# Kernel optimization log

Hardware: AMD Instinct MI355X
Metric: run time of the kernel (lower is better)

## Reference

```python
import jax, jax.numpy as jnp
import numpy as np

D_K = 64

def setup_inputs() -> dict:
    key = jax.random.key(0)
    kq, kk, kv, kw = jax.random.split(key, 4)
    B, H, L, Dk, Dv = 16, 8, 1024, 64, 64
    Q = jax.random.normal(kq, (B, H, L, Dk), dtype=jnp.float32)
    K = jax.random.normal(kk, (B, H, L, Dk), dtype=jnp.float32)
    V = jax.random.normal(kv, (B, H, L, Dv), dtype=jnp.float32)
    W = jax.random.normal(kw, (H, L, 2 * Dk), dtype=jnp.float32)
    return {"Q": Q, "K": K, "V": V, "W": W}

def reference(Q, K, V, W):
    scale = 1.0 / jnp.sqrt(jnp.float32(D_K))
    # branch 1: standard scaled dot-product attention scores [B,H,Lq,Lk]
    scores = jnp.einsum('bhqd,bhkd->bhqk', Q, K) * scale
    attn = jax.nn.softmax(scores, axis=-1)
    # branch 2: learned-weight concat(Q,K) projection
    # W [H, Lq, 2Dk] @ cat(Q,K)^T [B,H,2Dk,Lk] -> [B,H,Lq,Lk]
    qk = jnp.concatenate([Q, K], axis=-1)  # [B,H,L,2Dk]
    scores_cat = jnp.einsum('hqc,bhkc->bhqk', W, qk) * scale
    attn_cat = jax.nn.softmax(scores_cat, axis=-1)
    attention = attn + attn_cat
    context = jnp.einsum('bhqk,bhkd->bhqd', attention, V)
    return context, attention
```

## Files before the change

### kernel.cpp

```cpp
#include <hip/hip_runtime.h>

#define L_SEQ 1024
#define DKV 64
#define NT 16

typedef float f32x4 __attribute__((ext_vector_type(4)));
typedef _Float16 f16x8 __attribute__((ext_vector_type(8)));
typedef _Float16 f16x4 __attribute__((ext_vector_type(4)));

#define QK_STRIDE 136
#define VT_STRIDE 72
#define ATT_STRIDE 72

__device__ __forceinline__ f32x4 mfma16(f16x8 a, f16x8 b, f32x4 c) {
    return __builtin_amdgcn_mfma_f32_16x16x32_f16(a, b, c, 0, 0, 0);
}

__device__ __forceinline__ float fast_exp2(float x) {
#if __has_builtin(__builtin_amdgcn_exp2f)
    return __builtin_amdgcn_exp2f(x);
#else
    return exp2f(x);
#endif
}

__global__ __launch_bounds__(256, 2)
void fused_dual_attn(const float* __restrict__ Qg, const float* __restrict__ Kg,
                     const float* __restrict__ Vg, const float* __restrict__ Wg,
                     float* __restrict__ out_ctx, float* __restrict__ out_att)
{
    __shared__ _Float16 qk_lds[64 * QK_STRIDE];
    __shared__ _Float16 vt_lds[64 * VT_STRIDE];
    __shared__ _Float16 att_lds[64 * ATT_STRIDE];

    const int tid  = (int)threadIdx.x;
    const int lane = tid & 63;
    const int w    = tid >> 6;
    const int wr   = w >> 1;
    const int wc   = w & 1;
    const int a    = lane & 15;
    const int g    = lane >> 4;

    const int bid = (int)blockIdx.x;
    const int sw  = (bid & 7) * 256 + (bid >> 3);
    const int bh  = sw >> 4;
    const int q0  = (sw & 15) * 64;
    const int h   = bh & 7;

    const float SCALE_L2 = 0.125f * 1.44269504088896340736f;

    const float* Qh = Qg + (size_t)bh * (L_SEQ * DKV);
    const float* Kh = Kg + (size_t)bh * (L_SEQ * DKV);
    const float* Vh = Vg + (size_t)bh * (L_SEQ * DKV);
    const float* Wh = Wg + (size_t)h * (L_SEQ * 2 * DKV);

    f16x8 qa[2][2];
    f16x8 wa[2][4];
#pragma unroll
    for (int fr = 0; fr < 2; ++fr) {
        const int q = q0 + wr * 32 + fr * 16 + a;
        const float* qrow = Qh + q * DKV;
        const float* wrow = Wh + q * (2 * DKV);
#pragma unroll
        for (int kk = 0; kk < 2; ++kk) {
            const float* p = qrow + kk * 32 + g * 8;
            f32x4 lo = *(const f32x4*)p;
            f32x4 hi = *(const f32x4*)(p + 4);
            f16x8 v;
#pragma unroll
            for (int e = 0; e < 4; ++e) {
                v[e]     = (_Float16)(lo[e] * SCALE_L2);
                v[e + 4] = (_Float16)(hi[e] * SCALE_L2);
            }
            qa[fr][kk] = v;
        }
#pragma unroll
        for (int kk = 0; kk < 4; ++kk) {
            const float* p = wrow + kk * 32 + g * 8;
            f32x4 lo = *(const f32x4*)p;
            f32x4 hi = *(const f32x4*)(p + 4);
            f16x8 v;
#pragma unroll
            for (int e = 0; e < 4; ++e) {
                v[e]     = (_Float16)(lo[e] * SCALE_L2);
                v[e + 4] = (_Float16)(hi[e] * SCALE_L2);
            }
            wa[fr][kk] = v;
        }
    }

    auto stage_qk = [&](int t) {
#pragma unroll
        for (int i = 0; i < 8; ++i) {
            int u   = tid + i * 256;
            int row = u >> 5;
            int c   = (u & 31) * 4;
            const float* src = (c < 64) ? (Qh + (t * 64 + row) * DKV + c)
                                        : (Kh + (t * 64 + row) * DKV + (c - 64));
            f32x4 x = *(const f32x4*)src;
            f16x4 y;
#pragma unroll
            for (int e = 0; e < 4; ++e) y[e] = (_Float16)x[e];
            *(f16x4*)&qk_lds[row * QK_STRIDE + c] = y;
        }
    };

    auto stage_vt = [&](int t) {
        const int kq = tid >> 4;
        const int dc = tid & 15;
        const float* base = Vh + (t * 64 + 4 * kq) * DKV + 4 * dc;
        f32x4 r0 = *(const f32x4*)(base);
        f32x4 r1 = *(const f32x4*)(base + DKV);
        f32x4 r2 = *(const f32x4*)(base + 2 * DKV);
        f32x4 r3 = *(const f32x4*)(base + 3 * DKV);
#pragma unroll
        for (int i = 0; i < 4; ++i) {
            f16x4 y = { (_Float16)r0[i], (_Float16)r1[i], (_Float16)r2[i], (_Float16)r3[i] };
            *(f16x4*)&vt_lds[(4 * dc + i) * VT_STRIDE + 4 * kq] = y;
        }
    };

    auto compute_scores = [&](f32x4 (&s1)[2][2], f32x4 (&s2)[2][2]) {
        f16x8 kb[2][2], qb[2][2];
#pragma unroll
        for (int fc = 0; fc < 2; ++fc) {
            const int kp = wc * 32 + fc * 16 + a;
            const _Float16* rowp = &qk_lds[kp * QK_STRIDE];
#pragma unroll
            for (int kk = 0; kk < 2; ++kk) {
                qb[fc][kk] = *(const f16x8*)(rowp + kk * 32 + g * 8);
                kb[fc][kk] = *(const f16x8*)(rowp + 64 + kk * 32 + g * 8);
            }
        }
        const f32x4 cinit = { -13.0f, -13.0f, -13.0f, -13.0f };
#pragma unroll
        for (int fr = 0; fr < 2; ++fr) {
#pragma unroll
            for (int fc = 0; fc < 2; ++fc) {
                f32x4 acc = cinit;
                acc = mfma16(qa[fr][0], kb[fc][0], acc);
                acc = mfma16(qa[fr][1], kb[fc][1], acc);
                s1[fr][fc] = acc;
                f32x4 acc2 = cinit;
                acc2 = mfma16(wa[fr][0], qb[fc][0], acc2);
                acc2 = mfma16(wa[fr][1], qb[fc][1], acc2);
                acc2 = mfma16(wa[fr][2], kb[fc][0], acc2);
                acc2 = mfma16(wa[fr][3], kb[fc][1], acc2);
                s2[fr][fc] = acc2;
            }
        }
    };

    float lsum1[2][4] = {{0.f,0.f,0.f,0.f},{0.f,0.f,0.f,0.f}};
    float lsum2[2][4] = {{0.f,0.f,0.f,0.f},{0.f,0.f,0.f,0.f}};
    for (int t = 0; t < NT; ++t) {
        __syncthreads();
        stage_qk(t);
        __syncthreads();
        f32x4 s1[2][2], s2[2][2];
        compute_scores(s1, s2);
#pragma unroll
        for (int fr = 0; fr < 2; ++fr)
#pragma unroll
            for (int r = 0; r < 4; ++r) {
                lsum1[fr][r] += fast_exp2(s1[fr][0][r]) + fast_exp2(s1[fr][1][r]);
                lsum2[fr][r] += fast_exp2(s2[fr][0][r]) + fast_exp2(s2[fr][1][r]);
            }
    }

#pragma unroll
    for (int fr = 0; fr < 2; ++fr)
#pragma unroll
        for (int r = 0; r < 4; ++r) {
#pragma unroll
            for (int m = 1; m <= 8; m <<= 1) {
                lsum1[fr][r] += __shfl_xor(lsum1[fr][r], m, 64);
                lsum2[fr][r] += __shfl_xor(lsum2[fr][r], m, 64);
            }
        }

    float rinv1[2][4], rinv2[2][4];
    {
        float* sbuf = (float*)qk_lds;
        __syncthreads();
        if (a == 0) {
#pragma unroll
            for (int fr = 0; fr < 2; ++fr)
#pragma unroll
                for (int r = 0; r < 4; ++r) {
                    sbuf[w * 64 + fr * 16 + 4 * g + r]      = lsum1[fr][r];
                    sbuf[w * 64 + 32 + fr * 16 + 4 * g + r] = lsum2[fr][r];
                }
        }
        __syncthreads();
        const int pw = w ^ 1;
#pragma unroll
        for (int fr = 0; fr < 2; ++fr)
#pragma unroll
            for (int r = 0; r < 4; ++r) {
                float t1 = lsum1[fr][r] + sbuf[pw * 64 + fr * 16 + 4 * g + r];
                float t2 = lsum2[fr][r] + sbuf[pw * 64 + 32 + fr * 16 + 4 * g + r];
                rinv1[fr][r] = 1.0f / t1;
                rinv2[fr][r] = 1.0f / t2;
            }
    }

    f32x4 ctx[2][2] = {{{0.f,0.f,0.f,0.f},{0.f,0.f,0.f,0.f}},
                       {{0.f,0.f,0.f,0.f},{0.f,0.f,0.f,0.f}}};
    float* att_base = out_att + (size_t)bh * L_SEQ * L_SEQ;
    for (int t = 0; t < NT; ++t) {
        __syncthreads();
        stage_qk(t);
        stage_vt(t);
        __syncthreads();
        f32x4 s1[2][2], s2[2][2];
        compute_scores(s1, s2);
#pragma unroll
        for (int fr = 0; fr < 2; ++fr)
#pragma unroll
            for (int fc = 0; fc < 2; ++fc) {
                const int kl = wc * 32 + fc * 16 + a;
                const int kp = t * 64 + kl;
#pragma unroll
                for (int r = 0; r < 4; ++r) {
                    const int ql = wr * 32 + fr * 16 + 4 * g + r;
                    float av = fast_exp2(s1[fr][fc][r]) * rinv1[fr][r]
                             + fast_exp2(s2[fr][fc][r]) * rinv2[fr][r];
                    att_base[(size_t)(q0 + ql) * L_SEQ + kp] = av;
                    att_lds[ql * ATT_STRIDE + kl] = (_Float16)av;
                }
            }
        __syncthreads();
#pragma unroll
        for (int kk = 0; kk < 2; ++kk) {
            f16x8 pa0 = *(const f16x8*)&att_lds[(wr * 32 + a) * ATT_STRIDE + kk * 32 + g * 8];
            f16x8 pa1 = *(const f16x8*)&att_lds[(wr * 32 + 16 + a) * ATT_STRIDE + kk * 32 + g * 8];
#pragma unroll
            for (int fc2 = 0; fc2 < 2; ++fc2) {
                f16x8 vb = *(const f16x8*)&vt_lds[(wc * 32 + fc2 * 16 + a) * VT_STRIDE + kk * 32 + g * 8];
                ctx[0][fc2] = mfma16(pa0, vb, ctx[0][fc2]);
                ctx[1][fc2] = mfma16(pa1, vb, ctx[1][fc2]);
            }
        }
    }

    float* ctx_base = out_ctx + (size_t)bh * L_SEQ * DKV;
#pragma unroll
    for (int fr = 0; fr < 2; ++fr)
#pragma unroll
        for (int fc2 = 0; fc2 < 2; ++fc2)
#pragma unroll
            for (int r = 0; r < 4; ++r) {
                const int q = q0 + wr * 32 + fr * 16 + 4 * g + r;
                const int d = wc * 32 + fc2 * 16 + a;
                ctx_base[(size_t)q * DKV + d] = ctx[fr][fc2][r];
            }
}

extern "C" void kernel_launch(void* const* d_in, const int* in_sizes, int n_in,
                              void* d_out, int out_size, void* d_ws, size_t ws_size,
                              hipStream_t stream) {
    const float* Q = (const float*)d_in[0];
    const float* K = (const float*)d_in[1];
    const float* V = (const float*)d_in[2];
    const float* W = (const float*)d_in[3];
    float* out_ctx = (float*)d_out;
    float* out_att = out_ctx + (size_t)16 * 8 * 1024 * 64;
    fused_dual_attn<<<2048, 256, 0, stream>>>(Q, K, V, W, out_ctx, out_att);
}
```

Measured before the change: 861.0 us.

## Double-buffer K/Q/V tiles with register prefetch and per-wave row ownership

Each wave now owns 16 full query rows across all 64 keys instead of a 2x2 wave tiling. This removes the cross-wave LDS reduction of softmax sums and gives each wave a private attention LDS tile, so one barrier per tile iteration is dropped. Q/K and V tiles are prefetched into registers for the next iteration and stored into a second LDS buffer while the current one is consumed, hiding global load latency. The change also adds s_setprio around MFMA blocks and pads the LDS strides, at the cost of more LDS and register pressure that may lower occupancy.

```diff
diff --git a/kernel.cpp b/kernel.cpp
--- a/kernel.cpp
+++ b/kernel.cpp
@@ -9,8 +9,8 @@
 typedef _Float16 f16x4 __attribute__((ext_vector_type(4)));
 
 #define QK_STRIDE 136
-#define VT_STRIDE 72
-#define ATT_STRIDE 72
+#define VT_STRIDE 76
+#define ATT_STRIDE 80
 
 __device__ __forceinline__ f32x4 mfma16(f16x8 a, f16x8 b, f32x4 c) {
     return __builtin_amdgcn_mfma_f32_16x16x32_f16(a, b, c, 0, 0, 0);
@@ -29,15 +29,13 @@
                      const float* __restrict__ Vg, const float* __restrict__ Wg,
                      float* __restrict__ out_ctx, float* __restrict__ out_att)
 {
-    __shared__ _Float16 qk_lds[64 * QK_STRIDE];
-    __shared__ _Float16 vt_lds[64 * VT_STRIDE];
-    __shared__ _Float16 att_lds[64 * ATT_STRIDE];
+    __shared__ _Float16 qk_lds[2][64 * QK_STRIDE];
+    __shared__ _Float16 vt_lds[2][64 * VT_STRIDE];
+    __shared__ _Float16 att_lds[4][16 * ATT_STRIDE];
 
     const int tid  = (int)threadIdx.x;
     const int lane = tid & 63;
     const int w    = tid >> 6;
-    const int wr   = w >> 1;
-    const int wc   = w & 1;
     const int a    = lane & 15;
     const int g    = lane >> 4;
 
@@ -54,11 +52,10 @@
     const float* Vh = Vg + (size_t)bh * (L_SEQ * DKV);
     const float* Wh = Wg + (size_t)h * (L_SEQ * 2 * DKV);
 
-    f16x8 qa[2][2];
-    f16x8 wa[2][4];
-#pragma unroll
-    for (int fr = 0; fr < 2; ++fr) {
-        const int q = q0 + wr * 32 + fr * 16 + a;
+    f16x8 qa[2];
+    f16x8 wa[4];
+    {
+        const int q = q0 + w * 16 + a;
         const float* qrow = Qh + q * DKV;
         const float* wrow = Wh + q * (2 * DKV);
 #pragma unroll
@@ -72,7 +69,7 @@
                 v[e]     = (_Float16)(lo[e] * SCALE_L2);
                 v[e + 4] = (_Float16)(hi[e] * SCALE_L2);
             }
-            qa[fr][kk] = v;
+            qa[kk] = v;
         }
 #pragma unroll
         for (int kk = 0; kk < 4; ++kk) {
@@ -85,11 +82,12 @@
                 v[e]     = (_Float16)(lo[e] * SCALE_L2);
                 v[e + 4] = (_Float16)(hi[e] * SCALE_L2);
             }
-            wa[fr][kk] = v;
-        }
-    }
-
-    auto stage_qk = [&](int t) {
+            wa[kk] = v;
+        }
+    }
+
+    f32x4 qkreg[8];
+    auto qk_load = [&](int t) {
 #pragma unroll
         for (int i = 0; i < 8; ++i) {
             int u   = tid + i * 256;
@@ -97,35 +95,46 @@
             int c   = (u & 31) * 4;
             const float* src = (c < 64) ? (Qh + (t * 64 + row) * DKV + c)
                                         : (Kh + (t * 64 + row) * DKV + (c - 64));
-            f32x4 x = *(const f32x4*)src;
+            qkreg[i] = *(const f32x4*)src;
+        }
+    };
+    auto qk_store = [&](int b) {
+#pragma unroll
+        for (int i = 0; i < 8; ++i) {
+            int u   = tid + i * 256;
+            int row = u >> 5;
+            int c   = (u & 31) * 4;
             f16x4 y;
 #pragma unroll
-            for (int e = 0; e < 4; ++e) y[e] = (_Float16)x[e];
-            *(f16x4*)&qk_lds[row * QK_STRIDE + c] = y;
-        }
-    };
-
-    auto stage_vt = [&](int t) {
+            for (int e = 0; e < 4; ++e) y[e] = (_Float16)qkreg[i][e];
+            *(f16x4*)&qk_lds[b][row * QK_STRIDE + c] = y;
+        }
+    };
+
+    f32x4 vreg[4];
+    auto vt_load = [&](int t) {
         const int kq = tid >> 4;
         const int dc = tid & 15;
         const float* base = Vh + (t * 64 + 4 * kq) * DKV + 4 * dc;
-        f32x4 r0 = *(const f32x4*)(base);
-        f32x4 r1 = *(const f32x4*)(base + DKV);
-        f32x4 r2 = *(const f32x4*)(base + 2 * DKV);
-        f32x4 r3 = *(const f32x4*)(base + 3 * DKV);
+#pragma unroll
+        for (int j = 0; j < 4; ++j) vreg[j] = *(const f32x4*)(base + j * DKV);
+    };
+    auto vt_store = [&](int b) {
+        const int kq = tid >> 4;
+        const int dc = tid & 15;
 #pragma unroll
         for (int i = 0; i < 4; ++i) {
-            f16x4 y = { (_Float16)r0[i], (_Float16)r1[i], (_Float16)r2[i], (_Float16)r3[i] };
-            *(f16x4*)&vt_lds[(4 * dc + i) * VT_STRIDE + 4 * kq] = y;
-        }
-    };
-
-    auto compute_scores = [&](f32x4 (&s1)[2][2], f32x4 (&s2)[2][2]) {
-        f16x8 kb[2][2], qb[2][2];
-#pragma unroll
-        for (int fc = 0; fc < 2; ++fc) {
-            const int kp = wc * 32 + fc * 16 + a;
-            const _Float16* rowp = &qk_lds[kp * QK_STRIDE];
+            f16x4 y = { (_Float16)vreg[0][i], (_Float16)vreg[1][i],
+                        (_Float16)vreg[2][i], (_Float16)vreg[3][i] };
+            *(f16x4*)&vt_lds[b][(4 * dc + i) * VT_STRIDE + 4 * kq] = y;
+        }
+    };
+
+    auto compute_scores = [&](int b, f32x4 (&s1)[4], f32x4 (&s2)[4]) {
+        f16x8 kb[4][2], qb[4][2];
+#pragma unroll
+        for (int fc = 0; fc < 4; ++fc) {
+            const _Float16* rowp = &qk_lds[b][(fc * 16 + a) * QK_STRIDE];
 #pragma unroll
             for (int kk = 0; kk < 2; ++kk) {
                 qb[fc][kk] = *(const f16x8*)(rowp + kk * 32 + g * 8);
@@ -133,128 +142,103 @@
             }
         }
         const f32x4 cinit = { -13.0f, -13.0f, -13.0f, -13.0f };
-#pragma unroll
-        for (int fr = 0; fr < 2; ++fr) {
-#pragma unroll
-            for (int fc = 0; fc < 2; ++fc) {
-                f32x4 acc = cinit;
-                acc = mfma16(qa[fr][0], kb[fc][0], acc);
-                acc = mfma16(qa[fr][1], kb[fc][1], acc);
-                s1[fr][fc] = acc;
-                f32x4 acc2 = cinit;
-                acc2 = mfma16(wa[fr][0], qb[fc][0], acc2);
-                acc2 = mfma16(wa[fr][1], qb[fc][1], acc2);
-                acc2 = mfma16(wa[fr][2], kb[fc][0], acc2);
-                acc2 = mfma16(wa[fr][3], kb[fc][1], acc2);
-                s2[fr][fc] = acc2;
-            }
-        }
-    };
-
-    float lsum1[2][4] = {{0.f,0.f,0.f,0.f},{0.f,0.f,0.f,0.f}};
-    float lsum2[2][4] = {{0.f,0.f,0.f,0.f},{0.f,0.f,0.f,0.f}};
+        __builtin_amdgcn_s_setprio(1);
+#pragma unroll
+        for (int fc = 0; fc < 4; ++fc) {
+            f32x4 acc = cinit;
+            acc = mfma16(qa[0], kb[fc][0], acc);
+            acc = mfma16(qa[1], kb[fc][1], acc);
+            s1[fc] = acc;
+            f32x4 acc2 = cinit;
+            acc2 = mfma16(wa[0], qb[fc][0], acc2);
+            acc2 = mfma16(wa[1], qb[fc][1], acc2);
+            acc2 = mfma16(wa[2], kb[fc][0], acc2);
+            acc2 = mfma16(wa[3], kb[fc][1], acc2);
+            s2[fc] = acc2;
+        }
+        __builtin_amdgcn_s_setprio(0);
+    };
+
+    float lsum1[4] = {0.f, 0.f, 0.f, 0.f};
+    float lsum2[4] = {0.f, 0.f, 0.f, 0.f};
+    qk_load(0);
+    qk_store(0);
+    __syncthreads();
     for (int t = 0; t < NT; ++t) {
+        if (t < NT - 1) qk_load(t + 1);
+        f32x4 s1[4], s2[4];
+        compute_scores(t & 1, s1, s2);
+#pragma unroll
+        for (int fc = 0; fc < 4; ++fc)
+#pragma unroll
+            for (int r = 0; r < 4; ++r) {
+                lsum1[r] += fast_exp2(s1[fc][r]);
+                lsum2[r] += fast_exp2(s2[fc][r]);
+            }
+        if (t < NT - 1) qk_store((t + 1) & 1);
         __syncthreads();
-        stage_qk(t);
+    }
+
+    float rinv1[4], rinv2[4];
+#pragma unroll
+    for (int r = 0; r < 4; ++r) {
+#pragma unroll
+        for (int m = 1; m <= 8; m <<= 1) {
+            lsum1[r] += __shfl_xor(lsum1[r], m, 64);
+            lsum2[r] += __shfl_xor(lsum2[r], m, 64);
+        }
+        rinv1[r] = 1.0f / lsum1[r];
+        rinv2[r] = 1.0f / lsum2[r];
+    }
+
+    f32x4 ctx[4] = {{0.f,0.f,0.f,0.f},{0.f,0.f,0.f,0.f},
+                    {0.f,0.f,0.f,0.f},{0.f,0.f,0.f,0.f}};
+    float* att_base = out_att + (size_t)bh * L_SEQ * L_SEQ;
+    _Float16* patt = &att_lds[w][0];
+
+    qk_load(0);
+    vt_load(0);
+    qk_store(0);
+    vt_store(0);
+    __syncthreads();
+    for (int t = 0; t < NT; ++t) {
+        if (t < NT - 1) { qk_load(t + 1); vt_load(t + 1); }
+        f32x4 s1[4], s2[4];
+        compute_scores(t & 1, s1, s2);
+#pragma unroll
+        for (int fc = 0; fc < 4; ++fc)
+#pragma unroll
+            for (int r = 0; r < 4; ++r) {
+                const int ql = 4 * g + r;
+                float av = fast_exp2(s1[fc][r]) * rinv1[r]
+                         + fast_exp2(s2[fc][r]) * rinv2[r];
+                att_base[(size_t)(q0 + w * 16 + ql) * L_SEQ + t * 64 + fc * 16 + a] = av;
+                patt[ql * ATT_STRIDE + fc * 16 + a] = (_Float16)av;
+            }
+        __builtin_amdgcn_s_setprio(1);
+#pragma unroll
+        for (int kk = 0; kk < 2; ++kk) {
+            f16x8 pa = *(const f16x8*)&patt[a * ATT_STRIDE + kk * 32 + g * 8];
+#pragma unroll
+            for (int fc2 = 0; fc2 < 4; ++fc2) {
+                f16x8 vb = *(const f16x8*)&vt_lds[t & 1][(fc2 * 16 + a) * VT_STRIDE + kk * 32 + g * 8];
+                ctx[fc2] = mfma16(pa, vb, ctx[fc2]);
+            }
+        }
+        __builtin_amdgcn_s_setprio(0);
+        if (t < NT - 1) { qk_store((t + 1) & 1); vt_store((t + 1) & 1); }
         __syncthreads();
-        f32x4 s1[2][2], s2[2][2];
-        compute_scores(s1, s2);
-#pragma unroll
-        for (int fr = 0; fr < 2; ++fr)
-#pragma unroll
-            for (int r = 0; r < 4; ++r) {
-                lsum1[fr][r] += fast_exp2(s1[fr][0][r]) + fast_exp2(s1[fr][1][r]);
-                lsum2[fr][r] += fast_exp2(s2[fr][0][r]) + fast_exp2(s2[fr][1][r]);
-            }
-    }
-
-#pragma unroll
-    for (int fr = 0; fr < 2; ++fr)
+    }
+
+    float* ctx_base = out_ctx + (size_t)bh * L_SEQ * DKV;
+#pragma unroll
+    for (int fc2 = 0; fc2 < 4; ++fc2)
 #pragma unroll
         for (int r = 0; r < 4; ++r) {
-#pragma unroll
-            for (int m = 1; m <= 8; m <<= 1) {
-                lsum1[fr][r] += __shfl_xor(lsum1[fr][r], m, 64);
-                lsum2[fr][r] += __shfl_xor(lsum2[fr][r], m, 64);
-            }
-        }
-
-    float rinv1[2][4], rinv2[2][4];
-    {
-        float* sbuf = (float*)qk_lds;
-        __syncthreads();
-        if (a == 0) {
-#pragma unroll
-            for (int fr = 0; fr < 2; ++fr)
-#pragma unroll
-                for (int r = 0; r < 4; ++r) {
-                    sbuf[w * 64 + fr * 16 + 4 * g + r]      = lsum1[fr][r];
-                    sbuf[w * 64 + 32 + fr * 16 + 4 * g + r] = lsum2[fr][r];
-                }
-        }
-        __syncthreads();
-        const int pw = w ^ 1;
-#pragma unroll
-        for (int fr = 0; fr < 2; ++fr)
-#pragma unroll
-            for (int r = 0; r < 4; ++r) {
-                float t1 = lsum1[fr][r] + sbuf[pw * 64 + fr * 16 + 4 * g + r];
-                float t2 = lsum2[fr][r] + sbuf[pw * 64 + 32 + fr * 16 + 4 * g + r];
-                rinv1[fr][r] = 1.0f / t1;
-                rinv2[fr][r] = 1.0f / t2;
-            }
-    }
-
-    f32x4 ctx[2][2] = {{{0.f,0.f,0.f,0.f},{0.f,0.f,0.f,0.f}},
-                       {{0.f,0.f,0.f,0.f},{0.f,0.f,0.f,0.f}}};
-    float* att_base = out_att + (size_t)bh * L_SEQ * L_SEQ;
-    for (int t = 0; t < NT; ++t) {
-        __syncthreads();
-        stage_qk(t);
-        stage_vt(t);
-        __syncthreads();
-        f32x4 s1[2][2], s2[2][2];
-        compute_scores(s1, s2);
-#pragma unroll
-        for (int fr = 0; fr < 2; ++fr)
-#pragma unroll
-            for (int fc = 0; fc < 2; ++fc) {
-                const int kl = wc * 32 + fc * 16 + a;
-                const int kp = t * 64 + kl;
-#pragma unroll
-                for (int r = 0; r < 4; ++r) {
-                    const int ql = wr * 32 + fr * 16 + 4 * g + r;
-                    float av = fast_exp2(s1[fr][fc][r]) * rinv1[fr][r]
-                             + fast_exp2(s2[fr][fc][r]) * rinv2[fr][r];
-                    att_base[(size_t)(q0 + ql) * L_SEQ + kp] = av;
-                    att_lds[ql * ATT_STRIDE + kl] = (_Float16)av;
-                }
-            }
-        __syncthreads();
-#pragma unroll
-        for (int kk = 0; kk < 2; ++kk) {
-            f16x8 pa0 = *(const f16x8*)&att_lds[(wr * 32 + a) * ATT_STRIDE + kk * 32 + g * 8];
-            f16x8 pa1 = *(const f16x8*)&att_lds[(wr * 32 + 16 + a) * ATT_STRIDE + kk * 32 + g * 8];
-#pragma unroll
-            for (int fc2 = 0; fc2 < 2; ++fc2) {
-                f16x8 vb = *(const f16x8*)&vt_lds[(wc * 32 + fc2 * 16 + a) * VT_STRIDE + kk * 32 + g * 8];
-                ctx[0][fc2] = mfma16(pa0, vb, ctx[0][fc2]);
-                ctx[1][fc2] = mfma16(pa1, vb, ctx[1][fc2]);
-            }
-        }
-    }
-
-    float* ctx_base = out_ctx + (size_t)bh * L_SEQ * DKV;
-#pragma unroll
-    for (int fr = 0; fr < 2; ++fr)
-#pragma unroll
-        for (int fc2 = 0; fc2 < 2; ++fc2)
-#pragma unroll
-            for (int r = 0; r < 4; ++r) {
-                const int q = q0 + wr * 32 + fr * 16 + 4 * g + r;
-                const int d = wc * 32 + fc2 * 16 + a;
-                ctx_base[(size_t)q * DKV + d] = ctx[fr][fc2][r];
-            }
+            const int q = q0 + w * 16 + 4 * g + r;
+            const int d = fc2 * 16 + a;
+            ctx_base[(size_t)q * DKV + d] = ctx[fc2][r];
+        }
 }
 
 extern "C" void kernel_launch(void* const* d_in, const int* in_sizes, int n_in,
```

Result: faster. 802.8 us (-6.8%).
